# Kernel tuning notes

Measured on AMD Instinct MI355X. Metric: run time of the kernel, lower is better.

Reference implementation:

```python
import jax, jax.numpy as jnp
import numpy as np

N_NODES = 100000
N_EDGES = 1600000
D_INPUT = 128
D_HIDDEN = 16
N_HEADS = 8
NCLASSES = 40
N_GRAPHS = 64
ALPHA = 0.2  # LeakyReLU negative slope
INIT = 0.01  # GAT_param_init uniform range


def setup_inputs() -> dict:
    key = jax.random.key(0)
    ks = jax.random.split(key, 7)
    x = jax.random.normal(ks[0], (N_NODES, D_INPUT), dtype=jnp.float32)
    edge_idx = jax.random.randint(ks[1], (2, N_EDGES), 0, N_NODES, dtype=jnp.int64)
    batch = jnp.sort(jax.random.randint(ks[2], (N_NODES,), 0, N_GRAPHS, dtype=jnp.int64))
    # layer1: d_input -> n_heads * d_hidden, concat aggregate
    W1 = jax.random.uniform(ks[3], (D_INPUT, N_HEADS * D_HIDDEN), dtype=jnp.float32, minval=-INIT, maxval=INIT)
    a1 = jax.random.uniform(ks[4], (N_HEADS, 2 * D_HIDDEN), dtype=jnp.float32, minval=-INIT, maxval=INIT)
    # layer2: n_heads*d_hidden -> nclasses, 1 head, mean aggregate
    W2 = jax.random.uniform(ks[5], (N_HEADS * D_HIDDEN, NCLASSES), dtype=jnp.float32, minval=-INIT, maxval=INIT)
    a2 = jax.random.uniform(ks[6], (1, 2 * NCLASSES), dtype=jnp.float32, minval=-INIT, maxval=INIT)
    return {"x": x, "W1": W1, "a1": a1, "W2": W2, "a2": a2, "edge_idx": edge_idx, "batch": batch}


def _gat_layer(x, W, a, n_heads, d_out, src, dst, aggregate):
    # x: [N, d_in]; W: [d_in, H*D]; a: [H, 2*D]
    n = x.shape[0]
    Wh = (x @ W).reshape(n, n_heads, d_out)                  # [N, H, D]
    e_src = jnp.einsum('nhd,hd->nh', Wh, a[:, :d_out])       # [N, H]
    e_dst = jnp.einsum('nhd,hd->nh', Wh, a[:, d_out:])       # [N, H]
    e = jax.nn.leaky_relu(e_src[src] + e_dst[dst], ALPHA)    # [E, H]
    # segment softmax over edges sharing the same destination node
    m = jax.ops.segment_max(e, dst, num_segments=n)          # [N, H]
    m = jnp.where(jnp.isfinite(m), m, 0.0)                   # nodes w/o in-edges
    ex = jnp.exp(e - m[dst])
    s = jax.ops.segment_sum(ex, dst, num_segments=n)
    att = ex / (s[dst] + 1e-16)                              # [E, H]
    # weighted scatter-aggregate of neighbor features
    out = jax.ops.segment_sum(att[:, :, None] * Wh[src], dst, num_segments=n)  # [N, H, D]
    if aggregate == 'concat':
        return out.reshape(n, n_heads * d_out)
    return out.mean(axis=1)


def reference(x, W1, a1, W2, a2, edge_idx, batch):
    # eval mode: F.dropout(training=False) is identity
    src, dst = edge_idx[0], edge_idx[1]
    h1 = _gat_layer(x, W1, a1, N_HEADS, D_HIDDEN, src, dst, 'concat')
    h1 = jax.nn.elu(h1)
    h2 = _gat_layer(h1, W2, a2, 1, NCLASSES, src, dst, 'mean')   # [N, nclasses]
    # global_mean_pool over graph ids
    sums = jax.ops.segment_sum(h2, batch, num_segments=N_GRAPHS)
    cnt = jax.ops.segment_sum(jnp.ones((h2.shape[0],), h2.dtype), batch, num_segments=N_GRAPHS)
    return sums / jnp.maximum(cnt, 1.0)[:, None]
```

## Files before the change

### kernel.cpp

```cpp
#include <hip/hip_runtime.h>
#include <hip/hip_bf16.h>

typedef unsigned short u16;
typedef unsigned int   u32;
typedef float f32x2 __attribute__((ext_vector_type(2)));
typedef float f32x4 __attribute__((ext_vector_type(4)));
typedef short bf16x8 __attribute__((ext_vector_type(8)));

static constexpr int NN = 100000;
static constexpr int NE = 1600000;
static constexpr int NG = 64;

static constexpr int BSH   = 8;
static constexpr int NBUCK = 391;
static constexpr int BCAP  = 5120;
static constexpr int PB    = 8;

__device__ __forceinline__ u16 bf16rte(float a) {
  u32 u = __builtin_bit_cast(u32, a);
  u = (u + 0x7FFFu + ((u >> 16) & 1u)) >> 16;
  return (u16)u;
}
__device__ __forceinline__ u32 bf16pair(float a, float b) {
  return (u32)bf16rte(a) | ((u32)bf16rte(b) << 16);
}
__device__ __forceinline__ float bflo(u32 u) { return __builtin_bit_cast(float, u << 16); }
__device__ __forceinline__ float bfhi(u32 u) { return __builtin_bit_cast(float, u & 0xFFFF0000u); }

__device__ __forceinline__ void pkfma(f32x2& a, f32x2 w2, u32 u) {
  f32x2 v;
  v.x = bflo(u); v.y = bfhi(u);
  asm("v_pk_fma_f32 %0, %1, %2, %0" : "+v"(a) : "v"(w2), "v"(v));
}

__global__ void k_prep(const float* __restrict__ W1, u16* __restrict__ wsTg,
                       const int* __restrict__ batch, int* __restrict__ gstart) {
  const int bid = blockIdx.x;
  if (bid < 64) {
    int idx = bid * 256 + threadIdx.x;
    int k = idx >> 7, c = idx & 127;
    wsTg[c * 128 + (((k >> 3) ^ (c & 7)) << 3) + (k & 7)] = bf16rte(W1[idx]);
  } else {
    int g = threadIdx.x;
    if (g <= NG) {
      int lo = 0, hi = NN;
      while (lo < hi) { int mid = (lo + hi) >> 1; if (batch[mid] < g) lo = mid + 1; else hi = mid; }
      gstart[g] = lo;
    }
  }
}

__global__ __launch_bounds__(256) void k_gemm1(
    const float* __restrict__ x, const u16* __restrict__ wsTg, const float* __restrict__ a1,
    u16* __restrict__ Wh1b, float* __restrict__ es1, float* __restrict__ ed1)
{
  __shared__ u16 wsT[128][128];
  __shared__ u16 xsb[64][32];
  const int t = threadIdx.x;
  const int w = t >> 6, l = t & 63;
  const int rowBase = blockIdx.x * 64;

  {
    const uint4* src = (const uint4*)wsTg;
    uint4* dst = (uint4*)&wsT[0][0];
#pragma unroll
    for (int i = 0; i < 8; ++i) dst[t * 8 + i] = src[t * 8 + i];
  }

  f32x4 acc[4][2];
#pragma unroll
  for (int r = 0; r < 4; ++r)
#pragma unroll
    for (int cf = 0; cf < 2; ++cf) acc[r][cf] = (f32x4){0.f, 0.f, 0.f, 0.f};

  const int rr = t >> 2, cg = t & 3;
  const int grow_s = rowBase + rr;

  for (int kk0 = 0; kk0 < 128; kk0 += 32) {
    float4 v0 = make_float4(0.f, 0.f, 0.f, 0.f), v1 = v0;
    if (grow_s < NN) {
      v0 = *(const float4*)(&x[(size_t)grow_s * 128 + kk0 + cg * 8]);
      v1 = *(const float4*)(&x[(size_t)grow_s * 128 + kk0 + cg * 8 + 4]);
    }
    if (kk0) __syncthreads();
    {
      u32 p0 = bf16pair(v0.x, v0.y);
      u32 p1 = bf16pair(v0.z, v0.w);
      u32 p2 = bf16pair(v1.x, v1.y);
      u32 p3 = bf16pair(v1.z, v1.w);
      int sg = cg ^ ((rr >> 1) & 3);
      *(uint4*)(&xsb[rr][sg * 8]) = make_uint4(p0, p1, p2, p3);
    }
    __syncthreads();

    bf16x8 bfr[2];
#pragma unroll
    for (int cf = 0; cf < 2; ++cf) {
      int col = w * 32 + cf * 16 + (l & 15);
      int kg = (kk0 >> 3) + (l >> 4);
      bfr[cf] = *(const bf16x8*)(&wsT[col][(kg ^ (col & 7)) * 8]);
    }
#pragma unroll
    for (int r = 0; r < 4; ++r) {
      int row = r * 16 + (l & 15);
      int kg = l >> 4;
      bf16x8 afr = *(const bf16x8*)(&xsb[row][(kg ^ ((row >> 1) & 3)) * 8]);
#pragma unroll
      for (int cf = 0; cf < 2; ++cf)
        acc[r][cf] = __builtin_amdgcn_mfma_f32_16x16x32_bf16(afr, bfr[cf], acc[r][cf], 0, 0, 0);
    }
  }

  const int cl = l & 15;
  const int rq = l >> 4;
#pragma unroll
  for (int cf = 0; cf < 2; ++cf) {
    const int h = w * 2 + cf;
    const int gcol = w * 32 + cf * 16 + cl;
    const float as = a1[h * 32 + cl];
    const float ad = a1[h * 32 + 16 + cl];
#pragma unroll
    for (int r = 0; r < 4; ++r) {
#pragma unroll
      for (int i = 0; i < 4; ++i) {
        int grow = rowBase + r * 16 + rq * 4 + i;
        float wh = acc[r][cf][i];
        float ps = wh * as, pd = wh * ad;
        ps += __shfl_xor(ps, 1); ps += __shfl_xor(ps, 2);
        ps += __shfl_xor(ps, 4); ps += __shfl_xor(ps, 8);
        pd += __shfl_xor(pd, 1); pd += __shfl_xor(pd, 2);
        pd += __shfl_xor(pd, 4); pd += __shfl_xor(pd, 8);
        if (grow < NN) {
          Wh1b[(size_t)grow * 128 + gcol] = bf16rte(wh);
          if (cl == 0) { es1[grow * 8 + h] = ps; ed1[grow * 8 + h] = pd; }
        }
      }
    }
  }
}

__global__ __launch_bounds__(256) void k_bin(
    const int* __restrict__ src, const int* __restrict__ dst,
    int* __restrict__ cur, u32* __restrict__ ebuf)
{
  __shared__ int lcnt[512];
  __shared__ int goff[NBUCK];
  __shared__ u32 bin[4096];
  const int t = threadIdx.x;
  const int e0 = blockIdx.x * 4096;

  lcnt[t] = 0; lcnt[t + 256] = 0;
  __syncthreads();

  u32 ent[16]; short bb[16], lp[16];
#pragma unroll
  for (int i = 0; i < 16; ++i) {
    int e = e0 + i * 256 + t;
    if (e < NE) {
      int s = src[e], d = dst[e];
      int b = d >> BSH;
      ent[i] = (u32)s | ((u32)(d & 255) << 20);
      bb[i] = (short)b;
      lp[i] = (short)atomicAdd(&lcnt[b], 1);
    } else bb[i] = -1;
  }
  __syncthreads();
  for (int d = 1; d < 512; d <<= 1) {
    int v0 = (t >= d) ? lcnt[t - d] : 0;
    int v1 = (t + 256 >= d) ? lcnt[t + 256 - d] : 0;
    __syncthreads();
    lcnt[t] += v0; lcnt[t + 256] += v1;
    __syncthreads();
  }
  for (int b = t; b < NBUCK; b += 256) {
    int excl = b ? lcnt[b - 1] : 0;
    int cnt = lcnt[b] - excl;
    if (cnt) goff[b] = b * BCAP + atomicAdd(&cur[b], cnt);
  }
#pragma unroll
  for (int i = 0; i < 16; ++i) {
    if (bb[i] >= 0) {
      int excl = bb[i] ? lcnt[bb[i] - 1] : 0;
      bin[excl + lp[i]] = ent[i];
    }
  }
  __syncthreads();
  const int total = lcnt[NBUCK - 1];
  for (int i = t; i < total; i += 256) {
    int lo = 0, hi = NBUCK - 1;
    while (lo < hi) { int mid = (lo + hi) >> 1; if (lcnt[mid] > i) hi = mid; else lo = mid + 1; }
    int excl = lo ? lcnt[lo - 1] : 0;
    int g = goff[lo] + (i - excl);
    if (g < (lo + 1) * BCAP) ebuf[g] = bin[i];
  }
}

__global__ __launch_bounds__(256) void k_sort(
    const int* __restrict__ cur, u32* __restrict__ ebuf,
    int* __restrict__ offs, int* __restrict__ deg)
{
  __shared__ u32 ein[BCAP];
  __shared__ u32 eout[BCAP];
  __shared__ int nd[256];
  __shared__ int ncur[256];
  const int t = threadIdx.x;
  const int b = blockIdx.x;
  const int base = b * BCAP;
  int cnt = cur[b];
  if (cnt > BCAP) cnt = BCAP;
  const int nloc = min(256, NN - (b << BSH));

  for (int i = t; i < cnt; i += 256) ein[i] = ebuf[base + i];
  nd[t] = 0;
  __syncthreads();
  for (int i = t; i < cnt; i += 256) atomicAdd(&nd[ein[i] >> 20], 1);
  __syncthreads();
  const int myCnt = nd[t];
  for (int d = 1; d < 256; d <<= 1) {
    int v = (t >= d) ? nd[t - d] : 0;
    __syncthreads();
    nd[t] += v;
    __syncthreads();
  }
  const int excl = t ? nd[t - 1] : 0;
  ncur[t] = excl;
  if (t < nloc) {
    int node = (b << BSH) + t;
    offs[node] = base + excl;
    deg[node]  = myCnt;
  }
  __syncthreads();
  for (int i = t; i < cnt; i += 256) {
    u32 v = ein[i];
    int pos = atomicAdd(&ncur[v >> 20], 1);
    eout[pos] = v & 0xFFFFFu;
  }
  __syncthreads();
  for (int i = t; i < cnt; i += 256) ebuf[base + i] = eout[i];
}

__global__ __launch_bounds__(256, 8) void k_agg1(
    const u16* __restrict__ Wh1b, const float* __restrict__ es1, const float* __restrict__ ed1,
    const int* __restrict__ offs, const int* __restrict__ deg, const int* __restrict__ csr,
    u16* __restrict__ h1b)
{
  const int wid = threadIdx.x >> 6;
  const int lane = threadIdx.x & 63;
  const int n = blockIdx.x * 4 + wid;
  if (n >= NN) return;
  const int s0 = offs[n];
  const int nE = deg[n];
  const int g = lane >> 4;
  const int db = lane & 15;
  const int h = db >> 1;
  const float edv = ed1[n * 8 + h];

  f32x2 acc[4];
#pragma unroll
  for (int i = 0; i < 4; ++i) { acc[i].x = 0.f; acc[i].y = 0.f; }
  float ssum = 0.f;

  int c0 = 0;
  for (; c0 + 16 <= nE; c0 += 16) {
    int ss[4];
#pragma unroll
    for (int q = 0; q < 4; ++q) ss[q] = csr[s0 + c0 + q * 4 + g];
    float zz[4];
#pragma unroll
    for (int q = 0; q < 4; ++q) {
      float z = es1[ss[q] * 8 + h] + edv;
      zz[q] = (z > 0.f) ? z : 0.2f * z;
    }
    uint4 raw[4];
#pragma unroll
    for (int q = 0; q < 4; ++q)
      raw[q] = *(const uint4*)(Wh1b + (size_t)ss[q] * 128 + db * 8);
#pragma unroll
    for (int q = 0; q < 4; ++q) {
      const float ww = __expf(zz[q]);
      ssum += ww;
      f32x2 w2; w2.x = ww; w2.y = ww;
      pkfma(acc[0], w2, raw[q].x);
      pkfma(acc[1], w2, raw[q].y);
      pkfma(acc[2], w2, raw[q].z);
      pkfma(acc[3], w2, raw[q].w);
    }
  }
  if (c0 < nE) {
    int jj[4], ss[4];
#pragma unroll
    for (int q = 0; q < 4; ++q) {
      jj[q] = c0 + q * 4 + g;
      ss[q] = csr[s0 + (jj[q] < nE ? jj[q] : 0)];
    }
    float zz[4];
#pragma unroll
    for (int q = 0; q < 4; ++q) {
      float z = es1[ss[q] * 8 + h] + edv;
      zz[q] = (z > 0.f) ? z : 0.2f * z;
    }
#pragma unroll
    for (int q = 0; q < 4; ++q) {
      if (jj[q] < nE) {
        const uint4 raw = *(const uint4*)(Wh1b + (size_t)ss[q] * 128 + db * 8);
        const float ww = __expf(zz[q]);
        ssum += ww;
        f32x2 w2; w2.x = ww; w2.y = ww;
        pkfma(acc[0], w2, raw.x);
        pkfma(acc[1], w2, raw.y);
        pkfma(acc[2], w2, raw.z);
        pkfma(acc[3], w2, raw.w);
      }
    }
  }
#pragma unroll
  for (int i = 0; i < 4; ++i) {
    acc[i].x += __shfl_xor(acc[i].x, 16);
    acc[i].y += __shfl_xor(acc[i].y, 16);
    acc[i].x += __shfl_xor(acc[i].x, 32);
    acc[i].y += __shfl_xor(acc[i].y, 32);
  }
  ssum += __shfl_xor(ssum, 16);
  ssum += __shfl_xor(ssum, 32);

  if (g == 0) {
    float inv = 1.f / (ssum + 1e-16f);
    float o[8];
#pragma unroll
    for (int i = 0; i < 4; ++i) {
      float v0 = acc[i].x * inv;
      float v1 = acc[i].y * inv;
      o[2 * i]     = (v0 > 0.f) ? v0 : expm1f(v0);
      o[2 * i + 1] = (v1 > 0.f) ? v1 : expm1f(v1);
    }
    u32 p0 = bf16pair(o[0], o[1]);
    u32 p1 = bf16pair(o[2], o[3]);
    u32 p2 = bf16pair(o[4], o[5]);
    u32 p3 = bf16pair(o[6], o[7]);
    *(uint4*)(h1b + (size_t)n * 128 + db * 8) = make_uint4(p0, p1, p2, p3);
  }
}

__global__ __launch_bounds__(256) void k_gemm2(
    const u16* __restrict__ h1b, const float* __restrict__ W2,
    const float* __restrict__ a2,
    u16* __restrict__ Wh2b, float* __restrict__ es2, float* __restrict__ ed2)
{
  __shared__ float hs[128][36];
  __shared__ float w2s[32][40];
  const int t = threadIdx.x;
  const int rowBase = blockIdx.x * 128;
  const int cg = t & 3;
  const int rs = t >> 2;
  float acc[2][10];
#pragma unroll
  for (int r = 0; r < 2; ++r)
#pragma unroll
    for (int j = 0; j < 10; ++j) acc[r][j] = 0.f;

  for (int k0 = 0; k0 < 128; k0 += 32) {
#pragma unroll
    for (int p = 0; p < 2; ++p) {
      int idx = (p * 256 + t) * 8;
      int rr = idx >> 5, cc = idx & 31;
      int grow = rowBase + rr;
      uint4 hv = make_uint4(0u, 0u, 0u, 0u);
      if (grow < NN) hv = *(const uint4*)(h1b + (size_t)grow * 128 + k0 + cc);
      float2* dst = (float2*)&hs[rr][cc];
      dst[0] = make_float2(bflo(hv.x), bfhi(hv.x));
      dst[1] = make_float2(bflo(hv.y), bfhi(hv.y));
      dst[2] = make_float2(bflo(hv.z), bfhi(hv.z));
      dst[3] = make_float2(bflo(hv.w), bfhi(hv.w));
    }
#pragma unroll
    for (int p = 0; p < 5; ++p) {
      int idx = p * 256 + t;
      int kk = idx / 40, cc = idx % 40;
      w2s[kk][cc] = W2[(size_t)(k0 + kk) * 40 + cc];
    }
    __syncthreads();
#pragma unroll
    for (int k = 0; k < 32; ++k) {
      float a0 = hs[rs][k], a1v = hs[rs + 64][k];
#pragma unroll
      for (int j = 0; j < 10; ++j) {
        float b = w2s[k][cg * 10 + j];
        acc[0][j] = fmaf(a0, b, acc[0][j]);
        acc[1][j] = fmaf(a1v, b, acc[1][j]);
      }
    }
    __syncthreads();
  }
  float a2s[10], a2d[10];
#pragma unroll
  for (int j = 0; j < 10; ++j) {
    a2s[j] = a2[cg * 10 + j];
    a2d[j] = a2[40 + cg * 10 + j];
  }
#pragma unroll
  for (int rr = 0; rr < 2; ++rr) {
    int grow = rowBase + rs + rr * 64;
    float pes = 0.f, ped = 0.f;
#pragma unroll
    for (int j = 0; j < 10; ++j) {
      float v = acc[rr][j];
      pes = fmaf(v, a2s[j], pes);
      ped = fmaf(v, a2d[j], ped);
    }
    if (grow < NN) {
      u32* dst = (u32*)(Wh2b + (size_t)grow * 48 + cg * 10);
      dst[0] = bf16pair(acc[rr][0], acc[rr][1]);
      dst[1] = bf16pair(acc[rr][2], acc[rr][3]);
      dst[2] = bf16pair(acc[rr][4], acc[rr][5]);
      dst[3] = bf16pair(acc[rr][6], acc[rr][7]);
      dst[4] = bf16pair(acc[rr][8], acc[rr][9]);
    }
    pes += __shfl_xor(pes, 1); pes += __shfl_xor(pes, 2);
    ped += __shfl_xor(ped, 1); ped += __shfl_xor(ped, 2);
    if (cg == 0 && grow < NN) { es2[grow] = pes; ed2[grow] = ped; }
  }
}

__global__ __launch_bounds__(256, 8) void k_agg2(
    const u16* __restrict__ Wh2b, const float* __restrict__ es2, const float* __restrict__ ed2,
    const int* __restrict__ offs, const int* __restrict__ deg, const int* __restrict__ csr,
    float* __restrict__ h2)
{
  __shared__ float red[4][64][5];
  const int wid = threadIdx.x >> 6;
  const int lane = threadIdx.x & 63;
  const int n = blockIdx.x * 4 + wid;
  if (n >= NN) return;
  const int s0 = offs[n];
  const int nE = deg[n];
  const float edv = ed2[n];
  int e6 = lane / 10;
  const int r10 = lane - e6 * 10;
  const bool act = lane < 60;
  if (e6 > 5) e6 = 5;

  f32x2 acc0, acc1;
  acc0.x = acc0.y = acc1.x = acc1.y = 0.f;
  float ssum = 0.f;

  for (int c0 = 0; c0 < nE; c0 += 24) {
    int jj[4], ss[4];
#pragma unroll
    for (int q = 0; q < 4; ++q) {
      jj[q] = c0 + q * 6 + e6;
      ss[q] = csr[s0 + (jj[q] < nE ? jj[q] : 0)];
    }
    float zz[4];
#pragma unroll
    for (int q = 0; q < 4; ++q) {
      float z = es2[ss[q]] + edv;
      zz[q] = (z > 0.f) ? z : 0.2f * z;
    }
#pragma unroll
    for (int q = 0; q < 4; ++q) {
      if (act && jj[q] < nE) {
        const uint2 raw = *(const uint2*)(Wh2b + (size_t)ss[q] * 48 + r10 * 4);
        const float ww = __expf(zz[q]);
        ssum += ww;
        f32x2 w2; w2.x = ww; w2.y = ww;
        pkfma(acc0, w2, raw.x);
        pkfma(acc1, w2, raw.y);
      }
    }
  }
  red[wid][lane][0] = acc0.x; red[wid][lane][1] = acc0.y;
  red[wid][lane][2] = acc1.x; red[wid][lane][3] = acc1.y;
  red[wid][lane][4] = ssum;
  __builtin_amdgcn_wave_barrier();
  if (lane < 40) {
    const int rb = lane >> 2, e = lane & 3;
    float a = 0.f, sm = 0.f;
#pragma unroll
    for (int g = 0; g < 6; ++g) {
      a  += red[wid][g * 10 + rb][e];
      sm += red[wid][g * 10][4];
    }
    h2[(size_t)n * 40 + lane] = a / (sm + 1e-16f);
  }
}

__global__ __launch_bounds__(256) void k_pool1(
    const float* __restrict__ h2, const int* __restrict__ gstart,
    float* __restrict__ partial)
{
  __shared__ float lds[25][10][4];
  const int g = blockIdx.x >> 3;
  const int p = blockIdx.x & 7;
  const int t = threadIdx.x;
  const int s0 = gstart[g], s1 = gstart[g + 1];
  const int len = s1 - s0;
  const int chunk = (len + PB - 1) / PB;
  const int start = s0 + p * chunk;
  const int end = min(start + chunk, s1);
  const int slot = t / 10, q = t - slot * 10;
  float4 acc = make_float4(0.f, 0.f, 0.f, 0.f);
  if (slot < 25) {
    for (int n = start + slot; n < end; n += 25) {
      const float4 v = *(const float4*)(&h2[(size_t)n * 40 + q * 4]);
      acc.x += v.x; acc.y += v.y; acc.z += v.z; acc.w += v.w;
    }
    lds[slot][q][0] = acc.x; lds[slot][q][1] = acc.y;
    lds[slot][q][2] = acc.z; lds[slot][q][3] = acc.w;
  }
  __syncthreads();
  if (t < 40) {
    const int qq = t >> 2, e = t & 3;
    float s = 0.f;
#pragma unroll
    for (int sl = 0; sl < 25; ++sl) s += lds[sl][qq][e];
    partial[(size_t)blockIdx.x * 40 + t] = s;
  }
}

__global__ void k_pool2(const float* __restrict__ partial, const int* __restrict__ gstart,
                        float* __restrict__ out)
{
  const int g = blockIdx.x;
  const int d = threadIdx.x;
  if (d >= 40) return;
  float s = 0.f;
#pragma unroll
  for (int p = 0; p < PB; ++p) s += partial[(size_t)(g * PB + p) * 40 + d];
  int cnt = gstart[g + 1] - gstart[g];
  if (cnt < 1) cnt = 1;
  out[g * 40 + d] = s / (float)cnt;
}

extern "C" void kernel_launch(void* const* d_in, const int* in_sizes, int n_in,
                              void* d_out, int out_size, void* d_ws, size_t ws_size,
                              hipStream_t stream)
{
  const float* x   = (const float*)d_in[0];
  const float* W1  = (const float*)d_in[1];
  const float* a1  = (const float*)d_in[2];
  const float* W2  = (const float*)d_in[3];
  const float* a2  = (const float*)d_in[4];
  const int* eidx  = (const int*)d_in[5];
  const int* batch = (const int*)d_in[6];
  float* out = (float*)d_out;

  char* ws = (char*)d_ws;
  u16*   Wh1b = (u16*)(ws + 0);
  u16*   Wh2b = (u16*)(ws + 0);
  float* h2   = (float*)(ws + 9600000);
  u16*   h1b  = (u16*)(ws + 25600000);
  float* es1  = (float*)(ws + 51200000);
  float* ed1  = (float*)(ws + 54400000);
  float* es2  = (float*)(ws + 57600000);
  float* ed2  = (float*)(ws + 58000000);
  u32*   ebuf = (u32*)(ws + 58400000);
  int*   offs = (int*)(ws + 66407680);
  int*   deg  = (int*)(ws + 66807680);
  int*   cur  = (int*)(ws + 67207680);
  int*   gstart = (int*)(ws + 67209728);
  float* partial = (float*)(ws + 67210240);
  u16*   wsTg = (u16*)(ws + 67292160);

  const int* esrc = eidx;
  const int* edst = eidx + NE;

  hipMemsetAsync(cur, 0, NBUCK * sizeof(int), stream);
  k_prep<<<65, 256, 0, stream>>>(W1, wsTg, batch, gstart);
  k_gemm1<<<(NN + 63) / 64, 256, 0, stream>>>(x, wsTg, a1, Wh1b, es1, ed1);
  k_bin<<<(NE + 4095) / 4096, 256, 0, stream>>>(esrc, edst, cur, ebuf);
  k_sort<<<NBUCK, 256, 0, stream>>>(cur, ebuf, offs, deg);
  k_agg1<<<(NN + 3) / 4, 256, 0, stream>>>(Wh1b, es1, ed1, offs, deg, (const int*)ebuf, h1b);
  k_gemm2<<<(NN + 127) / 128, 256, 0, stream>>>(h1b, W2, a2, Wh2b, es2, ed2);
  k_agg2<<<(NN + 3) / 4, 256, 0, stream>>>(Wh2b, es2, ed2, offs, deg, (const int*)ebuf, h2);
  k_pool1<<<NG * PB, 256, 0, stream>>>(h2, gstart, partial);
  k_pool2<<<NG, 64, 0, stream>>>(partial, gstart, out);
}
```

Measured before the change: 256.8 us.

## Store h2 in bf16, split bin LDS counters, fold memset into prep

The layer-2 aggregation output is now written as bf16 pairs instead of fp32, halving the bytes written by k_agg2 and read by k_pool1. k_bin splits its per-bucket LDS atomic counters into two copies, one per half-block, to reduce atomic contention, and merges them before the scan. The hipMemsetAsync of the bucket cursors is removed and the zeroing is done inside k_prep, saving one launch. Storing h2 in bf16 adds rounding error to the pooled output.

```diff
diff --git a/kernel.cpp b/kernel.cpp
--- a/kernel.cpp
+++ b/kernel.cpp
@@ -34,18 +34,20 @@
 }
 
 __global__ void k_prep(const float* __restrict__ W1, u16* __restrict__ wsTg,
-                       const int* __restrict__ batch, int* __restrict__ gstart) {
+                       const int* __restrict__ batch, int* __restrict__ gstart,
+                       int* __restrict__ cur) {
   const int bid = blockIdx.x;
   if (bid < 64) {
     int idx = bid * 256 + threadIdx.x;
     int k = idx >> 7, c = idx & 127;
     wsTg[c * 128 + (((k >> 3) ^ (c & 7)) << 3) + (k & 7)] = bf16rte(W1[idx]);
   } else {
-    int g = threadIdx.x;
-    if (g <= NG) {
+    int t = threadIdx.x;
+    for (int i = t; i < NBUCK; i += 256) cur[i] = 0;
+    if (t <= NG) {
       int lo = 0, hi = NN;
-      while (lo < hi) { int mid = (lo + hi) >> 1; if (batch[mid] < g) lo = mid + 1; else hi = mid; }
-      gstart[g] = lo;
+      while (lo < hi) { int mid = (lo + hi) >> 1; if (batch[mid] < t) lo = mid + 1; else hi = mid; }
+      gstart[t] = lo;
     }
   }
 }
@@ -143,13 +145,16 @@
     const int* __restrict__ src, const int* __restrict__ dst,
     int* __restrict__ cur, u32* __restrict__ ebuf)
 {
-  __shared__ int lcnt[512];
+  __shared__ int lcnt2[2][512];
+  __shared__ int scn[512];
   __shared__ int goff[NBUCK];
   __shared__ u32 bin[4096];
   const int t = threadIdx.x;
+  const int wp = (t >> 7) & 1;
   const int e0 = blockIdx.x * 4096;
 
-  lcnt[t] = 0; lcnt[t + 256] = 0;
+  lcnt2[0][t] = 0; lcnt2[0][t + 256] = 0;
+  lcnt2[1][t] = 0; lcnt2[1][t + 256] = 0;
   __syncthreads();
 
   u32 ent[16]; short bb[16], lp[16];
@@ -161,35 +166,40 @@
       int b = d >> BSH;
       ent[i] = (u32)s | ((u32)(d & 255) << 20);
       bb[i] = (short)b;
-      lp[i] = (short)atomicAdd(&lcnt[b], 1);
+      lp[i] = (short)atomicAdd(&lcnt2[wp][b], 1);
     } else bb[i] = -1;
   }
   __syncthreads();
+  scn[t] = lcnt2[0][t] + lcnt2[1][t];
+  scn[t + 256] = lcnt2[0][t + 256] + lcnt2[1][t + 256];
+  __syncthreads();
   for (int d = 1; d < 512; d <<= 1) {
-    int v0 = (t >= d) ? lcnt[t - d] : 0;
-    int v1 = (t + 256 >= d) ? lcnt[t + 256 - d] : 0;
-    __syncthreads();
-    lcnt[t] += v0; lcnt[t + 256] += v1;
+    int v0 = (t >= d) ? scn[t - d] : 0;
+    int v1 = (t + 256 >= d) ? scn[t + 256 - d] : 0;
+    __syncthreads();
+    scn[t] += v0; scn[t + 256] += v1;
     __syncthreads();
   }
   for (int b = t; b < NBUCK; b += 256) {
-    int excl = b ? lcnt[b - 1] : 0;
-    int cnt = lcnt[b] - excl;
+    int excl = b ? scn[b - 1] : 0;
+    int cnt = scn[b] - excl;
     if (cnt) goff[b] = b * BCAP + atomicAdd(&cur[b], cnt);
   }
 #pragma unroll
   for (int i = 0; i < 16; ++i) {
     if (bb[i] >= 0) {
-      int excl = bb[i] ? lcnt[bb[i] - 1] : 0;
-      bin[excl + lp[i]] = ent[i];
-    }
-  }
-  __syncthreads();
-  const int total = lcnt[NBUCK - 1];
+      int b = bb[i];
+      int excl = b ? scn[b - 1] : 0;
+      int pos = excl + (wp ? lcnt2[0][b] : 0) + lp[i];
+      bin[pos] = ent[i];
+    }
+  }
+  __syncthreads();
+  const int total = scn[NBUCK - 1];
   for (int i = t; i < total; i += 256) {
     int lo = 0, hi = NBUCK - 1;
-    while (lo < hi) { int mid = (lo + hi) >> 1; if (lcnt[mid] > i) hi = mid; else lo = mid + 1; }
-    int excl = lo ? lcnt[lo - 1] : 0;
+    while (lo < hi) { int mid = (lo + hi) >> 1; if (scn[mid] > i) hi = mid; else lo = mid + 1; }
+    int excl = lo ? scn[lo - 1] : 0;
     int g = goff[lo] + (i - excl);
     if (g < (lo + 1) * BCAP) ebuf[g] = bin[i];
   }
@@ -424,7 +434,7 @@
 __global__ __launch_bounds__(256, 8) void k_agg2(
     const u16* __restrict__ Wh2b, const float* __restrict__ es2, const float* __restrict__ ed2,
     const int* __restrict__ offs, const int* __restrict__ deg, const int* __restrict__ csr,
-    float* __restrict__ h2)
+    u32* __restrict__ h2b)
 {
   __shared__ float red[4][64][5];
   const int wid = threadIdx.x >> 6;
@@ -472,20 +482,23 @@
   red[wid][lane][2] = acc1.x; red[wid][lane][3] = acc1.y;
   red[wid][lane][4] = ssum;
   __builtin_amdgcn_wave_barrier();
-  if (lane < 40) {
-    const int rb = lane >> 2, e = lane & 3;
-    float a = 0.f, sm = 0.f;
+  if (lane < 20) {
+    const int rb = lane >> 1;
+    const int eA = (lane & 1) * 2;
+    float aA = 0.f, aB = 0.f, sm = 0.f;
 #pragma unroll
     for (int g = 0; g < 6; ++g) {
-      a  += red[wid][g * 10 + rb][e];
+      aA += red[wid][g * 10 + rb][eA];
+      aB += red[wid][g * 10 + rb][eA + 1];
       sm += red[wid][g * 10][4];
     }
-    h2[(size_t)n * 40 + lane] = a / (sm + 1e-16f);
+    float inv = 1.f / (sm + 1e-16f);
+    h2b[(size_t)n * 20 + lane] = bf16pair(aA * inv, aB * inv);
   }
 }
 
 __global__ __launch_bounds__(256) void k_pool1(
-    const float* __restrict__ h2, const int* __restrict__ gstart,
+    const u32* __restrict__ h2b, const int* __restrict__ gstart,
     float* __restrict__ partial)
 {
   __shared__ float lds[25][10][4];
@@ -501,8 +514,9 @@
   float4 acc = make_float4(0.f, 0.f, 0.f, 0.f);
   if (slot < 25) {
     for (int n = start + slot; n < end; n += 25) {
-      const float4 v = *(const float4*)(&h2[(size_t)n * 40 + q * 4]);
-      acc.x += v.x; acc.y += v.y; acc.z += v.z; acc.w += v.w;
+      const uint2 v = *(const uint2*)(&h2b[(size_t)n * 20 + q * 2]);
+      acc.x += bflo(v.x); acc.y += bfhi(v.x);
+      acc.z += bflo(v.y); acc.w += bfhi(v.y);
     }
     lds[slot][q][0] = acc.x; lds[slot][q][1] = acc.y;
     lds[slot][q][2] = acc.z; lds[slot][q][3] = acc.w;
@@ -547,7 +561,7 @@
   char* ws = (char*)d_ws;
   u16*   Wh1b = (u16*)(ws + 0);
   u16*   Wh2b = (u16*)(ws + 0);
-  float* h2   = (float*)(ws + 9600000);
+  u32*   h2b  = (u32*)(ws + 9600000);
   u16*   h1b  = (u16*)(ws + 25600000);
   float* es1  = (float*)(ws + 51200000);
   float* ed1  = (float*)(ws + 54400000);
@@ -564,14 +578,13 @@
   const int* esrc = eidx;
   const int* edst = eidx + NE;
 
-  hipMemsetAsync(cur, 0, NBUCK * sizeof(int), stream);
-  k_prep<<<65, 256, 0, stream>>>(W1, wsTg, batch, gstart);
+  k_prep<<<65, 256, 0, stream>>>(W1, wsTg, batch, gstart, cur);
   k_gemm1<<<(NN + 63) / 64, 256, 0, stream>>>(x, wsTg, a1, Wh1b, es1, ed1);
   k_bin<<<(NE + 4095) / 4096, 256, 0, stream>>>(esrc, edst, cur, ebuf);
   k_sort<<<NBUCK, 256, 0, stream>>>(cur, ebuf, offs, deg);
   k_agg1<<<(NN + 3) / 4, 256, 0, stream>>>(Wh1b, es1, ed1, offs, deg, (const int*)ebuf, h1b);
   k_gemm2<<<(NN + 127) / 128, 256, 0, stream>>>(h1b, W2, a2, Wh2b, es2, ed2);
-  k_agg2<<<(NN + 3) / 4, 256, 0, stream>>>(Wh2b, es2, ed2, offs, deg, (const int*)ebuf, h2);
-  k_pool1<<<NG * PB, 256, 0, stream>>>(h2, gstart, partial);
+  k_agg2<<<(NN + 3) / 4, 256, 0, stream>>>(Wh2b, es2, ed2, offs, deg, (const int*)ebuf, h2b);
+  k_pool1<<<NG * PB, 256, 0, stream>>>(h2b, gstart, partial);
   k_pool2<<<NG, 64, 0, stream>>>(partial, gstart, out);
 }
```

Measured after the change: 250.6 us. -2.4%, faster.
